# Kernel optimization log

Measured on AMD Instinct MI355X. Metric: run time of the kernel, lower is better.

The kernel has to match this reference:

```python
import jax, jax.numpy as jnp
import numpy as np

N, F, DE = 768, 64, 32
H0, H1, H2, OUT = 64, 64, 128, 1  # hidden_dim=[64,64,128], output_dim=1


def _mlp(x, Wa, ba, Wb, bb):
    # two Dense layers with relu, as in the repo's MLP
    h = jax.nn.relu(x @ Wa + ba)
    return jax.nn.relu(h @ Wb + bb)


def _edge_conv_e(A, x, e, Wa, ba, Wb, bb):
    # EdgeConvE: per-edge message MLP([x_i, x_j - x_i, e_ij]) aggregated
    # over neighbors j weighted by the (binary) adjacency.
    n = x.shape[0]
    xi = jnp.broadcast_to(x[:, None, :], (n, n, x.shape[1]))  # [N,N,F]
    xj = jnp.broadcast_to(x[None, :, :], (n, n, x.shape[1]))  # [N,N,F]
    feat = jnp.concatenate([xi, xj - xi, e], axis=-1)         # [N,N,2F+De]
    m = _mlp(feat, Wa, ba, Wb, bb)                            # [N,N,H]
    return jnp.einsum('ij,ijh->ih', A, m)                     # scatter-sum over j


def setup_inputs() -> dict:
    key = jax.random.key(0)
    ks = jax.random.split(key, 16)
    adj = (jax.random.uniform(ks[0], (N, N)) < 0.05).astype(jnp.float32)
    x = jax.random.normal(ks[1], (N, F), dtype=jnp.float32)
    e = jax.random.normal(ks[2], (N, N, DE), dtype=jnp.float32)
    s = 0.05
    d_in1 = 2 * F + DE          # 160
    d_in2 = 2 * H0 + DE         # 160
    return {
        'ajacency': adj,
        'node_features': x,
        'edge_attributes': e,
        'W1a': jax.random.normal(ks[3], (d_in1, H0)) * s, 'b1a': jnp.zeros((H0,)),
        'W1b': jax.random.normal(ks[4], (H0, H0)) * s,    'b1b': jnp.zeros((H0,)),
        'W2a': jax.random.normal(ks[5], (d_in2, H1)) * s, 'b2a': jnp.zeros((H1,)),
        'W2b': jax.random.normal(ks[6], (H1, H0)) * s,    'b2b': jnp.zeros((H0,)),
        'W3': jax.random.normal(ks[7], (H0, H2)) * s,     'b3': jnp.zeros((H2,)),
        'W4': jax.random.normal(ks[8], (H2, OUT)) * s,    'b4': jnp.zeros((OUT,)),
    }


def reference(ajacency, node_features, edge_attributes,
              W1a, b1a, W1b, b1b, W2a, b2a, W2b, b2b, W3, b3, W4, b4):
    x = _edge_conv_e(ajacency, node_features, edge_attributes, W1a, b1a, W1b, b1b)
    x = _edge_conv_e(ajacency, x, edge_attributes, W2a, b2a, W2b, b2b)
    x = jax.nn.relu(x @ W3 + b3)
    return jax.nn.sigmoid(x @ W4 + b4)  # [N, OUT]
```

## Files before the change

kernel.cpp:

```cpp
#include <hip/hip_runtime.h>
#include <math.h>


#define NN 768
#define FF 64
#define DE 32
#define HH 64
#define EPB 32
#define CGRID 1024
#define ECAP (NN * 128)

__global__ __launch_bounds__(256) void scan_uv_kernel(
    const float* __restrict__ A, const float* __restrict__ x,
    const float* __restrict__ W, const float* __restrict__ bias,
    int* __restrict__ gcnt, int* __restrict__ edges,
    float* __restrict__ U, float* __restrict__ V,
    float* __restrict__ x1, float* __restrict__ x2)
{
  const int i = blockIdx.x;
  const int tid = threadIdx.x;
  __shared__ int s_cnt, s_base;
  __shared__ int s_j[NN];
  __shared__ float sx[64];
  __shared__ float su[4][64], sv[4][64];

  if (tid == 0) s_cnt = 0;
  __syncthreads();
  if (tid < 64) sx[tid] = x[i * 64 + tid];
  for (int j = tid; j < NN; j += 256) {
    if (A[i * NN + j] != 0.0f) {
      int p = atomicAdd(&s_cnt, 1);
      s_j[p] = j;
    }
  }
  if (tid < 64) { x1[i * 64 + tid] = 0.0f; x2[i * 64 + tid] = 0.0f; }
  __syncthreads();

  {
    const int c = tid & 63, qr = tid >> 6;
    float u = 0.0f, v = 0.0f;
#pragma unroll
    for (int t = 0; t < 16; ++t) {
      const int d = qr * 16 + t;
      const float xv = sx[d];
      const float wxi = W[d * 64 + c];
      const float wxj = W[(64 + d) * 64 + c];
      u = fmaf(xv, wxi - wxj, u);
      v = fmaf(xv, wxj, v);
    }
    su[qr][c] = u; sv[qr][c] = v;
  }
  if (tid == 0) s_base = atomicAdd(gcnt, s_cnt);
  __syncthreads();

  if (tid < 64) {
    U[i * 64 + tid] = su[0][tid] + su[1][tid] + su[2][tid] + su[3][tid] + bias[tid];
    V[i * 64 + tid] = sv[0][tid] + sv[1][tid] + sv[2][tid] + sv[3][tid];
  }
  const int c = s_cnt, b = s_base;
  for (int t = tid; t < c; t += 256) edges[b + t] = (i << 10) | s_j[t];
}

__global__ __launch_bounds__(256, 4) void uv_kernel(
    const float* __restrict__ x, const float* __restrict__ W,
    const float* __restrict__ bias, float* __restrict__ U, float* __restrict__ V)
{
  const int tid = threadIdx.x;
  const int rr = tid >> 6, c = tid & 63;
  const int r = blockIdx.x * 4 + rr;
  __shared__ float sx[4][64];
  sx[rr][c] = x[r * 64 + c];
  __syncthreads();
  float u = bias[c], v = 0.0f;
#pragma unroll
  for (int d = 0; d < 64; ++d) {
    float xv = sx[rr][d];
    float wxi = W[d * 64 + c];
    float wxj = W[(64 + d) * 64 + c];
    u = fmaf(xv, wxi - wxj, u);
    v = fmaf(xv, wxj, v);
  }
  U[r * 64 + c] = u;
  V[r * 64 + c] = v;
}

__global__ void conv1_kernel(
    const int* __restrict__ gcnt, const int* __restrict__ edges,
    const float* __restrict__ U, const float* __restrict__ V,
    const float* __restrict__ e, const float* __restrict__ We1,
    const float* __restrict__ We2, const float* __restrict__ Wb,
    const float* __restrict__ bb, float* __restrict__ xout,
    float* __restrict__ ew2)
{
  const int tid = threadIdx.x, lane = tid & 63, wv = tid >> 6;
  const int M = gcnt[0];
  const int base = blockIdx.x * EPB;
  if (base >= M) return;
  const int nedge = min(EPB, M - base);

  __shared__ __align__(16) float sh1[EPB * HH];
  __shared__ int si[EPB];

  float w1e[DE], w2e[DE];
#pragma unroll
  for (int d = 0; d < DE; ++d) { w1e[d] = We1[d * HH + lane]; w2e[d] = We2[d * HH + lane]; }

  const int a0 = wv * 8;
#pragma unroll
  for (int t = 0; t < 8; ++t) {
    int m = base + a0 + t;
    const bool valid = m < M;
    m = valid ? m : M - 1;
    const int p = edges[m];
    const int i = p >> 10, j = p & 1023;
    float h = U[(i << 6) + lane] + V[(j << 6) + lane];
    float g = 0.0f;
    const float4* ep = (const float4*)(e + ((size_t)i * NN + j) * DE);
#pragma unroll
    for (int u = 0; u < 8; ++u) {
      float4 f = ep[u];
      h = fmaf(f.x, w1e[4 * u + 0], h);
      h = fmaf(f.y, w1e[4 * u + 1], h);
      h = fmaf(f.z, w1e[4 * u + 2], h);
      h = fmaf(f.w, w1e[4 * u + 3], h);
      g = fmaf(f.x, w2e[4 * u + 0], g);
      g = fmaf(f.y, w2e[4 * u + 1], g);
      g = fmaf(f.z, w2e[4 * u + 2], g);
      g = fmaf(f.w, w2e[4 * u + 3], g);
    }
    sh1[(a0 + t) * HH + lane] = fmaxf(h, 0.0f);
    if (valid) ew2[(size_t)m * HH + lane] = g;
    if (lane == 0) si[a0 + t] = i;
  }

  const int slice = lane >> 4, kk = lane & 15;
  const int k = wv * 16 + kk;
  float w2[16];
#pragma unroll
  for (int t = 0; t < 16; ++t) w2[t] = Wb[(slice * 16 + t) * HH + k];
  const float bias2 = bb[k];

  __syncthreads();

  float acc = 0.0f;
  int cur_i = -1;
  for (int t = 0; t < nedge; ++t) {
    const int i = si[t];
    const float4* hp = (const float4*)(sh1 + t * HH + slice * 16);
    float q = bias2;
#pragma unroll
    for (int u = 0; u < 4; ++u) {
      float4 h = hp[u];
      q = fmaf(h.x, w2[4 * u + 0], q);
      q = fmaf(h.y, w2[4 * u + 1], q);
      q = fmaf(h.z, w2[4 * u + 2], q);
      q = fmaf(h.w, w2[4 * u + 3], q);
    }
    q += __shfl_down(q, 32);
    q += __shfl_down(q, 16);
    const float h2 = fmaxf(q, 0.0f);
    if (i != cur_i) {
      if (cur_i >= 0 && lane < 16) atomicAdd(&xout[(cur_i << 6) + k], acc);
      acc = 0.0f;
      cur_i = i;
    }
    acc += h2;
  }
  if (cur_i >= 0 && lane < 16) atomicAdd(&xout[(cur_i << 6) + k], acc);
}

__global__ void conv2_kernel(
    const int* __restrict__ gcnt, const int* __restrict__ edges,
    const float* __restrict__ U, const float* __restrict__ V,
    const float* __restrict__ ew2, const float* __restrict__ Wb,
    const float* __restrict__ bb, float* __restrict__ xout)
{
  const int tid = threadIdx.x, lane = tid & 63, wv = tid >> 6;
  const int M = gcnt[0];
  const int base = blockIdx.x * EPB;
  if (base >= M) return;
  const int nedge = min(EPB, M - base);

  __shared__ __align__(16) float sh1[EPB * HH];
  __shared__ int si[EPB];

  const int a0 = wv * 8;
#pragma unroll
  for (int t = 0; t < 8; ++t) {
    int m = base + a0 + t;
    m = m < M ? m : M - 1;
    const int p = edges[m];
    const int i = p >> 10, j = p & 1023;
    const float h = U[(i << 6) + lane] + V[(j << 6) + lane]
                  + ew2[(size_t)m * HH + lane];
    sh1[(a0 + t) * HH + lane] = fmaxf(h, 0.0f);
    if (lane == 0) si[a0 + t] = i;
  }

  const int slice = lane >> 4, kk = lane & 15;
  const int k = wv * 16 + kk;
  float w2[16];
#pragma unroll
  for (int t = 0; t < 16; ++t) w2[t] = Wb[(slice * 16 + t) * HH + k];
  const float bias2 = bb[k];

  __syncthreads();

  float acc = 0.0f;
  int cur_i = -1;
  for (int t = 0; t < nedge; ++t) {
    const int i = si[t];
    const float4* hp = (const float4*)(sh1 + t * HH + slice * 16);
    float q = bias2;
#pragma unroll
    for (int u = 0; u < 4; ++u) {
      float4 h = hp[u];
      q = fmaf(h.x, w2[4 * u + 0], q);
      q = fmaf(h.y, w2[4 * u + 1], q);
      q = fmaf(h.z, w2[4 * u + 2], q);
      q = fmaf(h.w, w2[4 * u + 3], q);
    }
    q += __shfl_down(q, 32);
    q += __shfl_down(q, 16);
    const float h2 = fmaxf(q, 0.0f);
    if (i != cur_i) {
      if (cur_i >= 0 && lane < 16) atomicAdd(&xout[(cur_i << 6) + k], acc);
      acc = 0.0f;
      cur_i = i;
    }
    acc += h2;
  }
  if (cur_i >= 0 && lane < 16) atomicAdd(&xout[(cur_i << 6) + k], acc);
}

__global__ __launch_bounds__(128) void final_kernel(
    const float* __restrict__ x2, const float* __restrict__ W3,
    const float* __restrict__ b3, const float* __restrict__ W4,
    const float* __restrict__ b4, float* __restrict__ out)
{
  const int i = blockIdx.x;
  const int t = threadIdx.x;
  const int lane = t & 63;
  const int wv = t >> 6;
  __shared__ float sx[64];
  __shared__ float s_red[2];
  if (t < 64) sx[t] = x2[i * 64 + t];
  __syncthreads();
  float p = b3[t];
#pragma unroll
  for (int c = 0; c < 64; ++c) p = fmaf(sx[c], W3[c * 128 + t], p);
  p = fmaxf(p, 0.0f);
  float v = p * W4[t];
  v += __shfl_down(v, 32);
  v += __shfl_down(v, 16);
  v += __shfl_down(v, 8);
  v += __shfl_down(v, 4);
  v += __shfl_down(v, 2);
  v += __shfl_down(v, 1);
  if (lane == 0) s_red[wv] = v;
  __syncthreads();
  if (t == 0) {
    float z = s_red[0] + s_red[1] + b4[0];
    out[i] = 1.0f / (1.0f + expf(-z));
  }
}

extern "C" void kernel_launch(void* const* d_in, const int* in_sizes, int n_in,
                              void* d_out, int out_size, void* d_ws, size_t ws_size,
                              hipStream_t stream) {
  const float* A   = (const float*)d_in[0];
  const float* x   = (const float*)d_in[1];
  const float* e   = (const float*)d_in[2];
  const float* W1a = (const float*)d_in[3];
  const float* b1a = (const float*)d_in[4];
  const float* W1b = (const float*)d_in[5];
  const float* b1b = (const float*)d_in[6];
  const float* W2a = (const float*)d_in[7];
  const float* b2a = (const float*)d_in[8];
  const float* W2b = (const float*)d_in[9];
  const float* b2b = (const float*)d_in[10];
  const float* W3  = (const float*)d_in[11];
  const float* b3  = (const float*)d_in[12];
  const float* W4  = (const float*)d_in[13];
  const float* b4  = (const float*)d_in[14];
  float* out = (float*)d_out;

  int*   gcnt  = (int*)d_ws;
  float* x1    = (float*)d_ws + 16;
  float* x2    = x1 + NN * HH;
  float* U1    = x2 + NN * HH;
  float* V1    = U1 + NN * HH;
  float* U2    = V1 + NN * HH;
  float* V2    = U2 + NN * HH;
  int*   edges = (int*)(V2 + NN * HH);
  float* ew2   = (float*)(edges + ECAP);

  hipMemsetAsync(gcnt, 0, 16 * sizeof(int), stream);

  scan_uv_kernel<<<NN, 256, 0, stream>>>(A, x, W1a, b1a, gcnt, edges, U1, V1, x1, x2);
  conv1_kernel<<<CGRID, 256, 0, stream>>>(gcnt, edges, U1, V1, e,
                                          W1a + 128 * HH, W2a + 128 * HH,
                                          W1b, b1b, x1, ew2);
  uv_kernel<<<NN / 4, 256, 0, stream>>>(x1, W2a, b2a, U2, V2);
  conv2_kernel<<<CGRID, 256, 0, stream>>>(gcnt, edges, U2, V2, ew2, W2b, b2b, x2);
  final_kernel<<<NN, 128, 0, stream>>>(x2, W3, b3, W4, b4, out);
}
```

Baseline: 181.3 us.

## Use bf16 MFMA for second edge-MLP layer with prepacked weights

Replaces the scalar FMA loop of the second dense layer in both conv kernels with bf16 16x16x32 MFMA instructions. Hidden activations are stored in shared memory as bf16 with a padded row stride. The Wb weights are converted once to a packed bf16 fragment layout inside the scan kernel. Per-edge scatter-add now happens from MFMA output registers. This cuts the FMA and shuffle work of phase B, at the cost of bf16 precision loss on activations and weights.

```diff
diff --git a/kernel.cpp b/kernel.cpp
--- a/kernel.cpp
+++ b/kernel.cpp
@@ -9,13 +9,24 @@
 #define EPB 32
 #define CGRID 1024
 #define ECAP (NN * 128)
+#define SH1S 72
+
+using bf16x8 = __attribute__((ext_vector_type(8))) short;
+using f32x4  = __attribute__((ext_vector_type(4))) float;
+
+__device__ __forceinline__ short f2b(float f) {
+  unsigned u = __float_as_uint(f);
+  return (short)((u + 0x7fffu + ((u >> 16) & 1u)) >> 16);
+}
 
 __global__ __launch_bounds__(256) void scan_uv_kernel(
     const float* __restrict__ A, const float* __restrict__ x,
     const float* __restrict__ W, const float* __restrict__ bias,
+    const float* __restrict__ Wb1, const float* __restrict__ Wb2,
     int* __restrict__ gcnt, int* __restrict__ edges,
     float* __restrict__ U, float* __restrict__ V,
-    float* __restrict__ x1, float* __restrict__ x2)
+    float* __restrict__ x1, float* __restrict__ x2,
+    short* __restrict__ Wbp1, short* __restrict__ Wbp2)
 {
   const int i = blockIdx.x;
   const int tid = threadIdx.x;
@@ -34,6 +45,16 @@
     }
   }
   if (tid < 64) { x1[i * 64 + tid] = 0.0f; x2[i * 64 + tid] = 0.0f; }
+
+  if (i < 2) {
+    const float* src = (i == 0) ? Wb1 : Wb2;
+    short* dst = (i == 0) ? Wbp1 : Wbp2;
+    for (int L = tid; L < 4096; L += 256) {
+      const int j = L & 7, n = (L >> 3) & 15, quad = (L >> 7) & 3;
+      const int kb = (L >> 9) & 1, ct = L >> 10;
+      dst[L] = f2b(src[(kb * 32 + quad * 8 + j) * 64 + ct * 16 + n]);
+    }
+  }
   __syncthreads();
 
   {
@@ -84,11 +105,62 @@
   V[r * 64 + c] = v;
 }
 
+__device__ __forceinline__ void phaseB_mfma(
+    const short* __restrict__ sh1b, const int* __restrict__ si,
+    const short* __restrict__ Wbp, const float* __restrict__ bb,
+    float* __restrict__ xout, int lane, int wv, int nedge)
+{
+  const int q = lane >> 4, n = lane & 15;
+  const int rt = wv >> 1;
+  const int ctbase = (wv & 1) * 2;
+
+  bf16x8 bf00 = *(const bf16x8*)(Wbp + ((((ctbase + 0) * 2 + 0) * 4 + q) * 16 + n) * 8);
+  bf16x8 bf01 = *(const bf16x8*)(Wbp + ((((ctbase + 0) * 2 + 1) * 4 + q) * 16 + n) * 8);
+  bf16x8 bf10 = *(const bf16x8*)(Wbp + ((((ctbase + 1) * 2 + 0) * 4 + q) * 16 + n) * 8);
+  bf16x8 bf11 = *(const bf16x8*)(Wbp + ((((ctbase + 1) * 2 + 1) * 4 + q) * 16 + n) * 8);
+  const float bias0 = bb[(ctbase + 0) * 16 + n];
+  const float bias1 = bb[(ctbase + 1) * 16 + n];
+
+  const short* sa = sh1b + (rt * 16 + n) * SH1S + q * 8;
+  bf16x8 a0 = *(const bf16x8*)(sa);
+  bf16x8 a1 = *(const bf16x8*)(sa + 32);
+
+  f32x4 acc0 = {0.f, 0.f, 0.f, 0.f}, acc1 = {0.f, 0.f, 0.f, 0.f};
+  acc0 = __builtin_amdgcn_mfma_f32_16x16x32_bf16(a0, bf00, acc0, 0, 0, 0);
+  acc0 = __builtin_amdgcn_mfma_f32_16x16x32_bf16(a1, bf01, acc0, 0, 0, 0);
+  acc1 = __builtin_amdgcn_mfma_f32_16x16x32_bf16(a0, bf10, acc1, 0, 0, 0);
+  acc1 = __builtin_amdgcn_mfma_f32_16x16x32_bf16(a1, bf11, acc1, 0, 0, 0);
+
+#pragma unroll
+  for (int c2 = 0; c2 < 2; ++c2) {
+    const f32x4 d = c2 ? acc1 : acc0;
+    const float bias = c2 ? bias1 : bias0;
+    const int ch = (ctbase + c2) * 16 + n;
+    float sum = 0.0f;
+    int cur = -1;
+#pragma unroll
+    for (int reg = 0; reg < 4; ++reg) {
+      const int t = rt * 16 + q * 4 + reg;
+      if (t < nedge) {
+        const int it = si[t];
+        const float v = fmaxf(d[reg] + bias, 0.0f);
+        if (it != cur) {
+          if (cur >= 0) atomicAdd(&xout[(cur << 6) + ch], sum);
+          sum = 0.0f;
+          cur = it;
+        }
+        sum += v;
+      }
+    }
+    if (cur >= 0) atomicAdd(&xout[(cur << 6) + ch], sum);
+  }
+}
+
 __global__ void conv1_kernel(
     const int* __restrict__ gcnt, const int* __restrict__ edges,
     const float* __restrict__ U, const float* __restrict__ V,
     const float* __restrict__ e, const float* __restrict__ We1,
-    const float* __restrict__ We2, const float* __restrict__ Wb,
+    const float* __restrict__ We2, const short* __restrict__ Wbp,
     const float* __restrict__ bb, float* __restrict__ xout,
     float* __restrict__ ew2)
 {
@@ -98,7 +170,7 @@
   if (base >= M) return;
   const int nedge = min(EPB, M - base);
 
-  __shared__ __align__(16) float sh1[EPB * HH];
+  __shared__ __align__(16) short sh1b[EPB * SH1S];
   __shared__ int si[EPB];
 
   float w1e[DE], w2e[DE];
@@ -128,51 +200,19 @@
       g = fmaf(f.z, w2e[4 * u + 2], g);
       g = fmaf(f.w, w2e[4 * u + 3], g);
     }
-    sh1[(a0 + t) * HH + lane] = fmaxf(h, 0.0f);
+    sh1b[(a0 + t) * SH1S + lane] = f2b(fmaxf(h, 0.0f));
     if (valid) ew2[(size_t)m * HH + lane] = g;
     if (lane == 0) si[a0 + t] = i;
   }
-
-  const int slice = lane >> 4, kk = lane & 15;
-  const int k = wv * 16 + kk;
-  float w2[16];
-#pragma unroll
-  for (int t = 0; t < 16; ++t) w2[t] = Wb[(slice * 16 + t) * HH + k];
-  const float bias2 = bb[k];
-
-  __syncthreads();
-
-  float acc = 0.0f;
-  int cur_i = -1;
-  for (int t = 0; t < nedge; ++t) {
-    const int i = si[t];
-    const float4* hp = (const float4*)(sh1 + t * HH + slice * 16);
-    float q = bias2;
-#pragma unroll
-    for (int u = 0; u < 4; ++u) {
-      float4 h = hp[u];
-      q = fmaf(h.x, w2[4 * u + 0], q);
-      q = fmaf(h.y, w2[4 * u + 1], q);
-      q = fmaf(h.z, w2[4 * u + 2], q);
-      q = fmaf(h.w, w2[4 * u + 3], q);
-    }
-    q += __shfl_down(q, 32);
-    q += __shfl_down(q, 16);
-    const float h2 = fmaxf(q, 0.0f);
-    if (i != cur_i) {
-      if (cur_i >= 0 && lane < 16) atomicAdd(&xout[(cur_i << 6) + k], acc);
-      acc = 0.0f;
-      cur_i = i;
-    }
-    acc += h2;
-  }
-  if (cur_i >= 0 && lane < 16) atomicAdd(&xout[(cur_i << 6) + k], acc);
+  __syncthreads();
+
+  phaseB_mfma(sh1b, si, Wbp, bb, xout, lane, wv, nedge);
 }
 
 __global__ void conv2_kernel(
     const int* __restrict__ gcnt, const int* __restrict__ edges,
     const float* __restrict__ U, const float* __restrict__ V,
-    const float* __restrict__ ew2, const float* __restrict__ Wb,
+    const float* __restrict__ ew2, const short* __restrict__ Wbp,
     const float* __restrict__ bb, float* __restrict__ xout)
 {
   const int tid = threadIdx.x, lane = tid & 63, wv = tid >> 6;
@@ -181,7 +221,7 @@
   if (base >= M) return;
   const int nedge = min(EPB, M - base);
 
-  __shared__ __align__(16) float sh1[EPB * HH];
+  __shared__ __align__(16) short sh1b[EPB * SH1S];
   __shared__ int si[EPB];
 
   const int a0 = wv * 8;
@@ -193,44 +233,12 @@
     const int i = p >> 10, j = p & 1023;
     const float h = U[(i << 6) + lane] + V[(j << 6) + lane]
                   + ew2[(size_t)m * HH + lane];
-    sh1[(a0 + t) * HH + lane] = fmaxf(h, 0.0f);
+    sh1b[(a0 + t) * SH1S + lane] = f2b(fmaxf(h, 0.0f));
     if (lane == 0) si[a0 + t] = i;
   }
-
-  const int slice = lane >> 4, kk = lane & 15;
-  const int k = wv * 16 + kk;
-  float w2[16];
-#pragma unroll
-  for (int t = 0; t < 16; ++t) w2[t] = Wb[(slice * 16 + t) * HH + k];
-  const float bias2 = bb[k];
-
-  __syncthreads();
-
-  float acc = 0.0f;
-  int cur_i = -1;
-  for (int t = 0; t < nedge; ++t) {
-    const int i = si[t];
-    const float4* hp = (const float4*)(sh1 + t * HH + slice * 16);
-    float q = bias2;
-#pragma unroll
-    for (int u = 0; u < 4; ++u) {
-      float4 h = hp[u];
-      q = fmaf(h.x, w2[4 * u + 0], q);
-      q = fmaf(h.y, w2[4 * u + 1], q);
-      q = fmaf(h.z, w2[4 * u + 2], q);
-      q = fmaf(h.w, w2[4 * u + 3], q);
-    }
-    q += __shfl_down(q, 32);
-    q += __shfl_down(q, 16);
-    const float h2 = fmaxf(q, 0.0f);
-    if (i != cur_i) {
-      if (cur_i >= 0 && lane < 16) atomicAdd(&xout[(cur_i << 6) + k], acc);
-      acc = 0.0f;
-      cur_i = i;
-    }
-    acc += h2;
-  }
-  if (cur_i >= 0 && lane < 16) atomicAdd(&xout[(cur_i << 6) + k], acc);
+  __syncthreads();
+
+  phaseB_mfma(sh1b, si, Wbp, bb, xout, lane, wv, nedge);
 }
 
 __global__ __launch_bounds__(128) void final_kernel(
@@ -294,14 +302,18 @@
   float* V2    = U2 + NN * HH;
   int*   edges = (int*)(V2 + NN * HH);
   float* ew2   = (float*)(edges + ECAP);
+  short* Wbp1  = (short*)(ew2 + (size_t)CGRID * EPB * HH);
+  short* Wbp2  = Wbp1 + 4096;
 
   hipMemsetAsync(gcnt, 0, 16 * sizeof(int), stream);
 
-  scan_uv_kernel<<<NN, 256, 0, stream>>>(A, x, W1a, b1a, gcnt, edges, U1, V1, x1, x2);
+  scan_uv_kernel<<<NN, 256, 0, stream>>>(A, x, W1a, b1a, W1b, W2b,
+                                         gcnt, edges, U1, V1, x1, x2, Wbp1, Wbp2);
   conv1_kernel<<<CGRID, 256, 0, stream>>>(gcnt, edges, U1, V1, e,
                                           W1a + 128 * HH, W2a + 128 * HH,
-                                          W1b, b1b, x1, ew2);
+                                          Wbp1, b1b, x1, ew2);
   uv_kernel<<<NN / 4, 256, 0, stream>>>(x1, W2a, b2a, U2, V2);
-  conv2_kernel<<<CGRID, 256, 0, stream>>>(gcnt, edges, U2, V2, ew2, W2b, b2b, x2);
+  conv2_kernel<<<CGRID, 256, 0, stream>>>(gcnt, edges, U2, V2, ew2,
+                                          Wbp2, b2b, x2);
   final_kernel<<<NN, 128, 0, stream>>>(x2, W3, b3, W4, b4, out);
 }
```

Result: no change. 179.1 us (-1.2%).
